# Performance work log

Measured on AMD Instinct MI355X. Metric: run time of the kernel, lower is better.

## Reference

```python
import jax, jax.numpy as jnp
import numpy as np

N_REGION = 50000
N_SUBJECT = 8192
D_REGION = 128
D_SUBJECT = 64
HIDDEN = 128
OUT = 64
E_RR = 1000000
E_HS = 400000


def setup_inputs() -> dict:
    key = jax.random.key(0)
    ks = jax.random.split(key, 18)
    w = lambda k, s: jax.random.normal(k, s, jnp.float32) * 0.05
    return {
        "x_region": jax.random.normal(ks[0], (N_REGION, D_REGION), jnp.float32),
        "x_subject": jax.random.normal(ks[1], (N_SUBJECT, D_SUBJECT), jnp.float32),
        "rr_src": jax.random.randint(ks[2], (E_RR,), 0, N_REGION, jnp.int32),
        "rr_dst": jax.random.randint(ks[3], (E_RR,), 0, N_REGION, jnp.int32),
        "hs_src": jax.random.randint(ks[4], (E_HS,), 0, N_REGION, jnp.int32),
        "hs_dst": jax.random.randint(ks[5], (E_HS,), 0, N_SUBJECT, jnp.int32),
        "Wg1": w(ks[6], (D_REGION, HIDDEN)), "bg1": w(ks[7], (HIDDEN,)),
        "Wl1": w(ks[8], (D_REGION, HIDDEN)), "bl1": w(ks[9], (HIDDEN,)),
        "Wr1": w(ks[10], (D_SUBJECT, HIDDEN)),
        "Wg2": w(ks[11], (HIDDEN, HIDDEN)), "bg2": w(ks[12], (HIDDEN,)),
        "Wl2": w(ks[13], (HIDDEN, HIDDEN)), "bl2": w(ks[14], (HIDDEN,)),
        "Wr2": w(ks[15], (HIDDEN, HIDDEN)),
        "Wout": w(ks[16], (HIDDEN, OUT)), "bout": w(ks[17], (OUT,)),
    }


def _gcn(x, src, dst, W, b, n):
    # GCNConv: symmetric normalization over A + I (add_self_loops=True)
    h = x @ W                                   # [n, hidden]
    deg = jnp.zeros((n,), x.dtype).at[dst].add(1.0) + 1.0  # in-degree + self-loop
    dinv = jax.lax.rsqrt(deg)
    norm = dinv[src] * dinv[dst]                # [E]
    out = jax.ops.segment_sum(h[src] * norm[:, None], dst, num_segments=n)
    return out + h / deg[:, None] + b           # self-loop term has norm 1/deg


def _sage(x_src, x_dst, src, dst, Wl, bl, Wr, n_dst):
    # SAGEConv: lin_l(mean_neighbors) + bias + lin_r(x_dst) (lin_r has no bias)
    s = jax.ops.segment_sum(x_src[src], dst, num_segments=n_dst)
    cnt = jax.ops.segment_sum(jnp.ones_like(src, dtype=x_src.dtype), dst, num_segments=n_dst)
    mean = s / jnp.maximum(cnt, 1.0)[:, None]
    return mean @ Wl + bl + x_dst @ Wr


def reference(x_region, x_subject, rr_src, rr_dst, hs_src, hs_dst,
              Wg1, bg1, Wl1, bl1, Wr1, Wg2, bg2, Wl2, bl2, Wr2, Wout, bout):
    # Layer 1 (HeteroConv applies both relations to the same input x_dict)
    r1 = _gcn(x_region, rr_src, rr_dst, Wg1, bg1, N_REGION)
    s1 = _sage(x_region, x_subject, hs_src, hs_dst, Wl1, bl1, Wr1, N_SUBJECT)
    # Layer 2
    r2 = _gcn(r1, rr_src, rr_dst, Wg2, bg2, N_REGION)
    s2 = _sage(r1, s1, hs_src, hs_dst, Wl2, bl2, Wr2, N_SUBJECT)
    # Final shared linear on each node type; concat (region rows, then subject rows)
    return jnp.concatenate([r2 @ Wout + bout, s2 @ Wout + bout], axis=0)
```

## Files before the change

### kernel.cpp

```cpp
#include <hip/hip_runtime.h>
#include <hip/hip_bf16.h>
#include <cstddef>

#define NR 50000
#define NS 8192
#define DR 128
#define DSUBJ 64
#define HID 128
#define OUTD 64
#define ERR_E 1000000
#define EHS_E 400000

__device__ inline int wave_incl_scan(int x, int lane) {
#pragma unroll
    for (int off = 1; off < 64; off <<= 1) {
        int t = __shfl_up(x, off, 64);
        if (lane >= off) x += t;
    }
    return x;
}

__global__ __launch_bounds__(256) void count_edges_both(const int* __restrict__ rr_dst,
                                                        const int* __restrict__ hs_dst,
                                                        int* __restrict__ rrCnt,
                                                        int* __restrict__ hsCnt) {
    int t = blockIdx.x * 256 + threadIdx.x;
    if (t < ERR_E) {
        atomicAdd(&rrCnt[rr_dst[t]], 1);
    } else {
        int u = t - ERR_E;
        if (u < EHS_E) atomicAdd(&hsCnt[hs_dst[u]], 1);
    }
}

__global__ __launch_bounds__(1024) void block_sums(const int* __restrict__ cnt,
                                                   int* __restrict__ partial, int n) {
    int tid = threadIdx.x, lane = tid & 63, wid = tid >> 6;
    int i = blockIdx.x * 1024 + tid;
    int v = (i < n) ? cnt[i] : 0;
    int s = v;
#pragma unroll
    for (int off = 1; off < 64; off <<= 1) s += __shfl_xor(s, off, 64);
    __shared__ int wsum[16];
    if (lane == 0) wsum[wid] = s;
    __syncthreads();
    if (tid == 0) {
        int tot = 0;
#pragma unroll
        for (int w = 0; w < 16; ++w) tot += wsum[w];
        partial[blockIdx.x] = tot;
    }
}

__global__ __launch_bounds__(64) void scan_partials(int* __restrict__ partial, int nb) {
    int lane = threadIdx.x;
    int v = (lane < nb) ? partial[lane] : 0;
    int incl = wave_incl_scan(v, lane);
    if (lane < nb) partial[lane] = incl - v;
}

template <int MODE>
__global__ __launch_bounds__(1024) void scan_finalize(int* __restrict__ cnt_cursor,
                                                      const int* __restrict__ partial,
                                                      int* __restrict__ rowptr,
                                                      float* __restrict__ scale, int n) {
    int tid = threadIdx.x, lane = tid & 63, wid = tid >> 6;
    int i = blockIdx.x * 1024 + tid;
    int v = (i < n) ? cnt_cursor[i] : 0;
    int incl = wave_incl_scan(v, lane);
    __shared__ int wsum[16];
    if (lane == 63) wsum[wid] = incl;
    __syncthreads();
    if (wid == 0 && lane < 16) {
        int orig = wsum[lane];
        int wv = orig;
#pragma unroll
        for (int off = 1; off < 16; off <<= 1) {
            int t = __shfl_up(wv, off, 64);
            if (lane >= off) wv += t;
        }
        wsum[lane] = wv - orig;
    }
    __syncthreads();
    int excl = partial[blockIdx.x] + wsum[wid] + incl - v;
    if (i < n) {
        rowptr[i + 1] = excl + v;
        cnt_cursor[i] = excl;
        if (MODE == 0) scale[i] = rsqrtf((float)(v + 1));
        else           scale[i] = 1.0f / fmaxf((float)v, 1.0f);
    }
    if (i == 0) rowptr[0] = 0;
}

__global__ __launch_bounds__(256) void fill_csr_both(const int* __restrict__ rr_src,
                                                     const int* __restrict__ rr_dst,
                                                     int* __restrict__ rrCursor,
                                                     int* __restrict__ rrCol,
                                                     const int* __restrict__ hs_src,
                                                     const int* __restrict__ hs_dst,
                                                     int* __restrict__ hsCursor,
                                                     int* __restrict__ hsCol) {
    int t = blockIdx.x * 256 + threadIdx.x;
    if (t < ERR_E) {
        int p = atomicAdd(&rrCursor[rr_dst[t]], 1);
        rrCol[p] = rr_src[t];
    } else {
        int u = t - ERR_E;
        if (u < EHS_E) {
            int p = atomicAdd(&hsCursor[hs_dst[u]], 1);
            hsCol[p] = hs_src[u];
        }
    }
}

template <int N, int K, bool BIAS, bool RS, bool ACCUM>
__global__ __launch_bounds__(256, 2) void gemm_lds(const float* __restrict__ A,
                                                   const float* __restrict__ W,
                                                   const float* __restrict__ bias,
                                                   const float* __restrict__ rs,
                                                   float* __restrict__ out, int M) {
    constexpr int CG = N / 4;
    constexpr int SLOTS = 256 / CG;
    constexpr int RPT = 64 / SLOTS;
    __shared__ float wl[K * N];

    for (int i = threadIdx.x * 4; i < K * N; i += 1024)
        *(float4*)&wl[i] = *(const float4*)&W[i];
    __syncthreads();

    int cg = threadIdx.x & (CG - 1);
    int rl = threadIdx.x / CG;
    int col = cg * 4;
    int row0 = blockIdx.x * 64 + rl * RPT;

    float4 acc[RPT];
#pragma unroll
    for (int j = 0; j < RPT; ++j) { acc[j].x = acc[j].y = acc[j].z = acc[j].w = 0.0f; }

#pragma unroll 2
    for (int k0 = 0; k0 < K; k0 += 4) {
        float4 a[RPT];
#pragma unroll
        for (int j = 0; j < RPT; ++j) {
            int r = row0 + j; if (r > M - 1) r = M - 1;
            a[j] = *(const float4*)(A + (size_t)r * K + k0);
        }
#pragma unroll
        for (int kk = 0; kk < 4; ++kk) {
            float4 w = *(float4*)&wl[(k0 + kk) * N + col];
#pragma unroll
            for (int j = 0; j < RPT; ++j) {
                float av = (kk == 0) ? a[j].x : (kk == 1) ? a[j].y : (kk == 2) ? a[j].z : a[j].w;
                acc[j].x += av * w.x;
                acc[j].y += av * w.y;
                acc[j].z += av * w.z;
                acc[j].w += av * w.w;
            }
        }
    }

    float4 b4;
    if (BIAS) b4 = *(const float4*)(bias + col);
#pragma unroll
    for (int j = 0; j < RPT; ++j) {
        int r = row0 + j;
        if (r >= M) continue;
        float4 v = acc[j];
        if (RS) { float sc = rs[r]; v.x *= sc; v.y *= sc; v.z *= sc; v.w *= sc; }
        if (BIAS) { v.x += b4.x; v.y += b4.y; v.z += b4.z; v.w += b4.w; }
        float* op = out + (size_t)r * N + col;
        if (ACCUM) {
            float4 o = *(const float4*)op;
            v.x += o.x; v.y += o.y; v.z += o.z; v.w += o.w;
        }
        *(float4*)op = v;
    }
}

__global__ __launch_bounds__(256) void gcn_gather(const float* __restrict__ h,
                                                  const int* __restrict__ rowptr,
                                                  const int* __restrict__ col,
                                                  const float* __restrict__ dinv,
                                                  const float* __restrict__ bias,
                                                  float* __restrict__ out, int n) {
    int wid = threadIdx.x >> 6;
    int lane = threadIdx.x & 63;
    int r = blockIdx.x * 4 + wid;
    if (r >= n) return;
    const float2* hp = (const float2*)h;
    float2 acc = hp[(size_t)r * 64 + lane];
    int e = rowptr[r], end = rowptr[r + 1];
    for (; e + 7 < end; e += 8) {
        int s0 = col[e],     s1 = col[e + 1], s2 = col[e + 2], s3 = col[e + 3];
        int s4 = col[e + 4], s5 = col[e + 5], s6 = col[e + 6], s7 = col[e + 7];
        float2 v0 = hp[(size_t)s0 * 64 + lane];
        float2 v1 = hp[(size_t)s1 * 64 + lane];
        float2 v2 = hp[(size_t)s2 * 64 + lane];
        float2 v3 = hp[(size_t)s3 * 64 + lane];
        float2 v4 = hp[(size_t)s4 * 64 + lane];
        float2 v5 = hp[(size_t)s5 * 64 + lane];
        float2 v6 = hp[(size_t)s6 * 64 + lane];
        float2 v7 = hp[(size_t)s7 * 64 + lane];
        acc.x += ((v0.x + v1.x) + (v2.x + v3.x)) + ((v4.x + v5.x) + (v6.x + v7.x));
        acc.y += ((v0.y + v1.y) + (v2.y + v3.y)) + ((v4.y + v5.y) + (v6.y + v7.y));
    }
    for (; e + 3 < end; e += 4) {
        int s0 = col[e], s1 = col[e + 1], s2 = col[e + 2], s3 = col[e + 3];
        float2 v0 = hp[(size_t)s0 * 64 + lane];
        float2 v1 = hp[(size_t)s1 * 64 + lane];
        float2 v2 = hp[(size_t)s2 * 64 + lane];
        float2 v3 = hp[(size_t)s3 * 64 + lane];
        acc.x += (v0.x + v1.x) + (v2.x + v3.x);
        acc.y += (v0.y + v1.y) + (v2.y + v3.y);
    }
    for (; e < end; ++e) {
        int s = col[e];
        float2 v = hp[(size_t)s * 64 + lane];
        acc.x += v.x; acc.y += v.y;
    }
    float dv = dinv[r];
    float2 b = ((const float2*)bias)[lane];
    acc.x = acc.x * dv + b.x;
    acc.y = acc.y * dv + b.y;
    ((float2*)out)[(size_t)r * 64 + lane] = acc;
}

__global__ __launch_bounds__(256) void sage_gather(const float* __restrict__ x,
                                                   const int* __restrict__ rowptr,
                                                   const int* __restrict__ col,
                                                   const float* __restrict__ invcnt,
                                                   float* __restrict__ out, int n) {
    int wid = threadIdx.x >> 6;
    int lane = threadIdx.x & 63;
    int r = blockIdx.x * 4 + wid;
    if (r >= n) return;
    const float2* xp = (const float2*)x;
    float2 acc; acc.x = 0.0f; acc.y = 0.0f;
    int e = rowptr[r], end = rowptr[r + 1];
    for (; e + 7 < end; e += 8) {
        int s0 = col[e],     s1 = col[e + 1], s2 = col[e + 2], s3 = col[e + 3];
        int s4 = col[e + 4], s5 = col[e + 5], s6 = col[e + 6], s7 = col[e + 7];
        float2 v0 = xp[(size_t)s0 * 64 + lane];
        float2 v1 = xp[(size_t)s1 * 64 + lane];
        float2 v2 = xp[(size_t)s2 * 64 + lane];
        float2 v3 = xp[(size_t)s3 * 64 + lane];
        float2 v4 = xp[(size_t)s4 * 64 + lane];
        float2 v5 = xp[(size_t)s5 * 64 + lane];
        float2 v6 = xp[(size_t)s6 * 64 + lane];
        float2 v7 = xp[(size_t)s7 * 64 + lane];
        acc.x += ((v0.x + v1.x) + (v2.x + v3.x)) + ((v4.x + v5.x) + (v6.x + v7.x));
        acc.y += ((v0.y + v1.y) + (v2.y + v3.y)) + ((v4.y + v5.y) + (v6.y + v7.y));
    }
    for (; e + 3 < end; e += 4) {
        int s0 = col[e], s1 = col[e + 1], s2 = col[e + 2], s3 = col[e + 3];
        float2 v0 = xp[(size_t)s0 * 64 + lane];
        float2 v1 = xp[(size_t)s1 * 64 + lane];
        float2 v2 = xp[(size_t)s2 * 64 + lane];
        float2 v3 = xp[(size_t)s3 * 64 + lane];
        acc.x += (v0.x + v1.x) + (v2.x + v3.x);
        acc.y += (v0.y + v1.y) + (v2.y + v3.y);
    }
    for (; e < end; ++e) {
        int s = col[e];
        float2 v = xp[(size_t)s * 64 + lane];
        acc.x += v.x; acc.y += v.y;
    }
    float ic = invcnt[r];
    acc.x *= ic; acc.y *= ic;
    ((float2*)out)[(size_t)r * 64 + lane] = acc;
}

extern "C" void kernel_launch(void* const* d_in, const int* in_sizes, int n_in,
                              void* d_out, int out_size, void* d_ws, size_t ws_size,
                              hipStream_t stream) {
    const float* x_region = (const float*)d_in[0];
    const float* x_subject = (const float*)d_in[1];
    const int* rr_src = (const int*)d_in[2];
    const int* rr_dst = (const int*)d_in[3];
    const int* hs_src = (const int*)d_in[4];
    const int* hs_dst = (const int*)d_in[5];
    const float* Wg1 = (const float*)d_in[6];
    const float* bg1 = (const float*)d_in[7];
    const float* Wl1 = (const float*)d_in[8];
    const float* bl1 = (const float*)d_in[9];
    const float* Wr1 = (const float*)d_in[10];
    const float* Wg2 = (const float*)d_in[11];
    const float* bg2 = (const float*)d_in[12];
    const float* Wl2 = (const float*)d_in[13];
    const float* bl2 = (const float*)d_in[14];
    const float* Wr2 = (const float*)d_in[15];
    const float* Wout = (const float*)d_in[16];
    const float* bout = (const float*)d_in[17];
    float* out = (float*)d_out;

    float* ws = (float*)d_ws;
    float* A  = ws;
    float* C  = A + (size_t)NR * 128;
    float* SA = C + (size_t)NR * 128;
    float* SB = SA + (size_t)NS * 128;
    float* SC = SB + (size_t)NS * 128;
    float* dinv   = SC + (size_t)NS * 128;
    float* invcnt = dinv + NR;
    int* rrRowptr = (int*)(invcnt + NS);
    int* rrCursor = rrRowptr + NR + 1;
    int* rrCol    = rrCursor + NR;
    int* hsRowptr = rrCol + ERR_E;
    int* hsCursor = hsRowptr + NS + 1;
    int* hsCol    = hsCursor + NS;
    int* rrPart   = hsCol + EHS_E;
    int* hsPart   = rrPart + 64;

    const int TB = 256;
    constexpr int RR_BLKS = (NR + 1023) / 1024;
    constexpr int HS_BLKS = (NS + 1023) / 1024;

    hipMemsetAsync(rrCursor, 0, (size_t)NR * sizeof(int), stream);
    hipMemsetAsync(hsCursor, 0, (size_t)NS * sizeof(int), stream);
    count_edges_both<<<(ERR_E + EHS_E + TB - 1) / TB, TB, 0, stream>>>(
        rr_dst, hs_dst, rrCursor, hsCursor);
    block_sums<<<RR_BLKS, 1024, 0, stream>>>(rrCursor, rrPart, NR);
    block_sums<<<HS_BLKS, 1024, 0, stream>>>(hsCursor, hsPart, NS);
    scan_partials<<<1, 64, 0, stream>>>(rrPart, RR_BLKS);
    scan_partials<<<1, 64, 0, stream>>>(hsPart, HS_BLKS);
    scan_finalize<0><<<RR_BLKS, 1024, 0, stream>>>(rrCursor, rrPart, rrRowptr, dinv, NR);
    scan_finalize<1><<<HS_BLKS, 1024, 0, stream>>>(hsCursor, hsPart, hsRowptr, invcnt, NS);
    fill_csr_both<<<(ERR_E + EHS_E + TB - 1) / TB, TB, 0, stream>>>(
        rr_src, rr_dst, rrCursor, rrCol, hs_src, hs_dst, hsCursor, hsCol);

    gemm_lds<128, 128, false, true, false><<<(NR + 63) / 64, TB, 0, stream>>>(
        x_region, Wg1, nullptr, dinv, A, NR);
    gcn_gather<<<(NR + 3) / 4, TB, 0, stream>>>(A, rrRowptr, rrCol, dinv, bg1, C, NR);
    sage_gather<<<(NS + 3) / 4, TB, 0, stream>>>(x_region, hsRowptr, hsCol, invcnt, SA, NS);
    gemm_lds<128, 128, true, false, false><<<(NS + 63) / 64, TB, 0, stream>>>(
        SA, Wl1, bl1, nullptr, SB, NS);
    gemm_lds<128, 64, false, false, true><<<(NS + 63) / 64, TB, 0, stream>>>(
        x_subject, Wr1, nullptr, nullptr, SB, NS);

    sage_gather<<<(NS + 3) / 4, TB, 0, stream>>>(C, hsRowptr, hsCol, invcnt, SA, NS);
    gemm_lds<128, 128, true, false, false><<<(NS + 63) / 64, TB, 0, stream>>>(
        SA, Wl2, bl2, nullptr, SC, NS);
    gemm_lds<128, 128, false, false, true><<<(NS + 63) / 64, TB, 0, stream>>>(
        SB, Wr2, nullptr, nullptr, SC, NS);
    gemm_lds<128, 128, false, true, false><<<(NR + 63) / 64, TB, 0, stream>>>(
        C, Wg2, nullptr, dinv, A, NR);
    gcn_gather<<<(NR + 3) / 4, TB, 0, stream>>>(A, rrRowptr, rrCol, dinv, bg2, C, NR);

    gemm_lds<64, 128, true, false, false><<<(NR + 63) / 64, TB, 0, stream>>>(
        C, Wout, bout, nullptr, out, NR);
    gemm_lds<64, 128, true, false, false><<<(NS + 63) / 64, TB, 0, stream>>>(
        SC, Wout, bout, nullptr, out + (size_t)NR * 64, NS);
}
```

Baseline: 689.1 us.

## Store gathered node features in bf16 to halve gather traffic

The GCN pre-aggregation GEMM now writes its output in bf16. Layer-1 GCN output gets a bf16 mirror, and x_region is cast to bf16 up front. Both gather kernels read these bf16 rows and accumulate in fp32, halving the bytes fetched per random edge access. The trade is lower precision on the aggregated features, plus an extra cast kernel and an extra mirror write.

```diff
diff --git a/kernel.cpp b/kernel.cpp
--- a/kernel.cpp
+++ b/kernel.cpp
@@ -10,6 +10,22 @@
 #define OUTD 64
 #define ERR_E 1000000
 #define EHS_E 400000
+
+typedef unsigned int uint32;
+typedef unsigned short ushort16;
+
+__device__ inline float bf16lo(uint32 u) { return __uint_as_float(u << 16); }
+__device__ inline float bf16hi(uint32 u) { return __uint_as_float(u & 0xffff0000u); }
+__device__ inline ushort16 f2bf(float f) {
+    uint32 u = __float_as_uint(f);
+    u += 0x7fffu + ((u >> 16) & 1u);
+    return (ushort16)(u >> 16);
+}
+__device__ inline uint32 pack2bf(float x, float y) {
+    uint32 ux = __float_as_uint(x); ux += 0x7fffu + ((ux >> 16) & 1u);
+    uint32 uy = __float_as_uint(y); uy += 0x7fffu + ((uy >> 16) & 1u);
+    return (ux >> 16) | (uy & 0xffff0000u);
+}
 
 __device__ inline int wave_incl_scan(int x, int lane) {
 #pragma unroll
@@ -113,7 +129,17 @@
     }
 }
 
-template <int N, int K, bool BIAS, bool RS, bool ACCUM>
+__global__ __launch_bounds__(256) void cast_bf(const float4* __restrict__ in,
+                                               ushort16* __restrict__ out, int n4) {
+    int i = blockIdx.x * 256 + threadIdx.x;
+    if (i < n4) {
+        float4 v = in[i];
+        ushort16* o = out + (size_t)i * 4;
+        o[0] = f2bf(v.x); o[1] = f2bf(v.y); o[2] = f2bf(v.z); o[3] = f2bf(v.w);
+    }
+}
+
+template <int N, int K, bool BIAS, bool RS, bool ACCUM, bool OB>
 __global__ __launch_bounds__(256, 2) void gemm_lds(const float* __restrict__ A,
                                                    const float* __restrict__ W,
                                                    const float* __restrict__ bias,
@@ -168,106 +194,118 @@
         float4 v = acc[j];
         if (RS) { float sc = rs[r]; v.x *= sc; v.y *= sc; v.z *= sc; v.w *= sc; }
         if (BIAS) { v.x += b4.x; v.y += b4.y; v.z += b4.z; v.w += b4.w; }
-        float* op = out + (size_t)r * N + col;
-        if (ACCUM) {
-            float4 o = *(const float4*)op;
-            v.x += o.x; v.y += o.y; v.z += o.z; v.w += o.w;
-        }
-        *(float4*)op = v;
-    }
-}
-
-__global__ __launch_bounds__(256) void gcn_gather(const float* __restrict__ h,
-                                                  const int* __restrict__ rowptr,
-                                                  const int* __restrict__ col,
-                                                  const float* __restrict__ dinv,
-                                                  const float* __restrict__ bias,
-                                                  float* __restrict__ out, int n) {
+        if (OB) {
+            uint32 lo = pack2bf(v.x, v.y);
+            uint32 hi = pack2bf(v.z, v.w);
+            uint32* op = (uint32*)((ushort16*)out + (size_t)r * N + col);
+            op[0] = lo; op[1] = hi;
+        } else {
+            float* op = out + (size_t)r * N + col;
+            if (ACCUM) {
+                float4 o = *(const float4*)op;
+                v.x += o.x; v.y += o.y; v.z += o.z; v.w += o.w;
+            }
+            *(float4*)op = v;
+        }
+    }
+}
+
+template <bool DUALW>
+__global__ __launch_bounds__(256) void gcn_gather_bf(const ushort16* __restrict__ h,
+                                                     const int* __restrict__ rowptr,
+                                                     const int* __restrict__ col,
+                                                     const float* __restrict__ dinv,
+                                                     const float* __restrict__ bias,
+                                                     float* __restrict__ out,
+                                                     ushort16* __restrict__ mirror, int n) {
     int wid = threadIdx.x >> 6;
     int lane = threadIdx.x & 63;
     int r = blockIdx.x * 4 + wid;
     if (r >= n) return;
-    const float2* hp = (const float2*)h;
-    float2 acc = hp[(size_t)r * 64 + lane];
+    const uint32* hp = (const uint32*)h;
+    uint32 us = hp[(size_t)r * 64 + lane];
+    float ax = bf16lo(us), ay = bf16hi(us);
     int e = rowptr[r], end = rowptr[r + 1];
     for (; e + 7 < end; e += 8) {
         int s0 = col[e],     s1 = col[e + 1], s2 = col[e + 2], s3 = col[e + 3];
         int s4 = col[e + 4], s5 = col[e + 5], s6 = col[e + 6], s7 = col[e + 7];
-        float2 v0 = hp[(size_t)s0 * 64 + lane];
-        float2 v1 = hp[(size_t)s1 * 64 + lane];
-        float2 v2 = hp[(size_t)s2 * 64 + lane];
-        float2 v3 = hp[(size_t)s3 * 64 + lane];
-        float2 v4 = hp[(size_t)s4 * 64 + lane];
-        float2 v5 = hp[(size_t)s5 * 64 + lane];
-        float2 v6 = hp[(size_t)s6 * 64 + lane];
-        float2 v7 = hp[(size_t)s7 * 64 + lane];
-        acc.x += ((v0.x + v1.x) + (v2.x + v3.x)) + ((v4.x + v5.x) + (v6.x + v7.x));
-        acc.y += ((v0.y + v1.y) + (v2.y + v3.y)) + ((v4.y + v5.y) + (v6.y + v7.y));
+        uint32 u0 = hp[(size_t)s0 * 64 + lane];
+        uint32 u1 = hp[(size_t)s1 * 64 + lane];
+        uint32 u2 = hp[(size_t)s2 * 64 + lane];
+        uint32 u3 = hp[(size_t)s3 * 64 + lane];
+        uint32 u4 = hp[(size_t)s4 * 64 + lane];
+        uint32 u5 = hp[(size_t)s5 * 64 + lane];
+        uint32 u6 = hp[(size_t)s6 * 64 + lane];
+        uint32 u7 = hp[(size_t)s7 * 64 + lane];
+        ax += ((bf16lo(u0) + bf16lo(u1)) + (bf16lo(u2) + bf16lo(u3)))
+            + ((bf16lo(u4) + bf16lo(u5)) + (bf16lo(u6) + bf16lo(u7)));
+        ay += ((bf16hi(u0) + bf16hi(u1)) + (bf16hi(u2) + bf16hi(u3)))
+            + ((bf16hi(u4) + bf16hi(u5)) + (bf16hi(u6) + bf16hi(u7)));
     }
     for (; e + 3 < end; e += 4) {
         int s0 = col[e], s1 = col[e + 1], s2 = col[e + 2], s3 = col[e + 3];
-        float2 v0 = hp[(size_t)s0 * 64 + lane];
-        float2 v1 = hp[(size_t)s1 * 64 + lane];
-        float2 v2 = hp[(size_t)s2 * 64 + lane];
-        float2 v3 = hp[(size_t)s3 * 64 + lane];
-        acc.x += (v0.x + v1.x) + (v2.x + v3.x);
-        acc.y += (v0.y + v1.y) + (v2.y + v3.y);
+        uint32 u0 = hp[(size_t)s0 * 64 + lane];
+        uint32 u1 = hp[(size_t)s1 * 64 + lane];
+        uint32 u2 = hp[(size_t)s2 * 64 + lane];
+        uint32 u3 = hp[(size_t)s3 * 64 + lane];
+        ax += (bf16lo(u0) + bf16lo(u1)) + (bf16lo(u2) + bf16lo(u3));
+        ay += (bf16hi(u0) + bf16hi(u1)) + (bf16hi(u2) + bf16hi(u3));
     }
     for (; e < end; ++e) {
-        int s = col[e];
-        float2 v = hp[(size_t)s * 64 + lane];
-        acc.x += v.x; acc.y += v.y;
+        uint32 u = hp[(size_t)col[e] * 64 + lane];
+        ax += bf16lo(u); ay += bf16hi(u);
     }
     float dv = dinv[r];
     float2 b = ((const float2*)bias)[lane];
-    acc.x = acc.x * dv + b.x;
-    acc.y = acc.y * dv + b.y;
-    ((float2*)out)[(size_t)r * 64 + lane] = acc;
-}
-
-__global__ __launch_bounds__(256) void sage_gather(const float* __restrict__ x,
-                                                   const int* __restrict__ rowptr,
-                                                   const int* __restrict__ col,
-                                                   const float* __restrict__ invcnt,
-                                                   float* __restrict__ out, int n) {
+    float ox = ax * dv + b.x;
+    float oy = ay * dv + b.y;
+    ((float2*)out)[(size_t)r * 64 + lane] = make_float2(ox, oy);
+    if (DUALW) ((uint32*)mirror)[(size_t)r * 64 + lane] = pack2bf(ox, oy);
+}
+
+__global__ __launch_bounds__(256) void sage_gather_bf(const ushort16* __restrict__ x,
+                                                      const int* __restrict__ rowptr,
+                                                      const int* __restrict__ col,
+                                                      const float* __restrict__ invcnt,
+                                                      float* __restrict__ out, int n) {
     int wid = threadIdx.x >> 6;
     int lane = threadIdx.x & 63;
     int r = blockIdx.x * 4 + wid;
     if (r >= n) return;
-    const float2* xp = (const float2*)x;
-    float2 acc; acc.x = 0.0f; acc.y = 0.0f;
+    const uint32* xp = (const uint32*)x;
+    float ax = 0.0f, ay = 0.0f;
     int e = rowptr[r], end = rowptr[r + 1];
     for (; e + 7 < end; e += 8) {
         int s0 = col[e],     s1 = col[e + 1], s2 = col[e + 2], s3 = col[e + 3];
         int s4 = col[e + 4], s5 = col[e + 5], s6 = col[e + 6], s7 = col[e + 7];
-        float2 v0 = xp[(size_t)s0 * 64 + lane];
-        float2 v1 = xp[(size_t)s1 * 64 + lane];
-        float2 v2 = xp[(size_t)s2 * 64 + lane];
-        float2 v3 = xp[(size_t)s3 * 64 + lane];
-        float2 v4 = xp[(size_t)s4 * 64 + lane];
-        float2 v5 = xp[(size_t)s5 * 64 + lane];
-        float2 v6 = xp[(size_t)s6 * 64 + lane];
-        float2 v7 = xp[(size_t)s7 * 64 + lane];
-        acc.x += ((v0.x + v1.x) + (v2.x + v3.x)) + ((v4.x + v5.x) + (v6.x + v7.x));
-        acc.y += ((v0.y + v1.y) + (v2.y + v3.y)) + ((v4.y + v5.y) + (v6.y + v7.y));
+        uint32 u0 = xp[(size_t)s0 * 64 + lane];
+        uint32 u1 = xp[(size_t)s1 * 64 + lane];
+        uint32 u2 = xp[(size_t)s2 * 64 + lane];
+        uint32 u3 = xp[(size_t)s3 * 64 + lane];
+        uint32 u4 = xp[(size_t)s4 * 64 + lane];
+        uint32 u5 = xp[(size_t)s5 * 64 + lane];
+        uint32 u6 = xp[(size_t)s6 * 64 + lane];
+        uint32 u7 = xp[(size_t)s7 * 64 + lane];
+        ax += ((bf16lo(u0) + bf16lo(u1)) + (bf16lo(u2) + bf16lo(u3)))
+            + ((bf16lo(u4) + bf16lo(u5)) + (bf16lo(u6) + bf16lo(u7)));
+        ay += ((bf16hi(u0) + bf16hi(u1)) + (bf16hi(u2) + bf16hi(u3)))
+            + ((bf16hi(u4) + bf16hi(u5)) + (bf16hi(u6) + bf16hi(u7)));
     }
     for (; e + 3 < end; e += 4) {
         int s0 = col[e], s1 = col[e + 1], s2 = col[e + 2], s3 = col[e + 3];
-        float2 v0 = xp[(size_t)s0 * 64 + lane];
-        float2 v1 = xp[(size_t)s1 * 64 + lane];
-        float2 v2 = xp[(size_t)s2 * 64 + lane];
-        float2 v3 = xp[(size_t)s3 * 64 + lane];
-        acc.x += (v0.x + v1.x) + (v2.x + v3.x);
-        acc.y += (v0.y + v1.y) + (v2.y + v3.y);
+        uint32 u0 = xp[(size_t)s0 * 64 + lane];
+        uint32 u1 = xp[(size_t)s1 * 64 + lane];
+        uint32 u2 = xp[(size_t)s2 * 64 + lane];
+        uint32 u3 = xp[(size_t)s3 * 64 + lane];
+        ax += (bf16lo(u0) + bf16lo(u1)) + (bf16lo(u2) + bf16lo(u3));
+        ay += (bf16hi(u0) + bf16hi(u1)) + (bf16hi(u2) + bf16hi(u3));
     }
     for (; e < end; ++e) {
-        int s = col[e];
-        float2 v = xp[(size_t)s * 64 + lane];
-        acc.x += v.x; acc.y += v.y;
+        uint32 u = xp[(size_t)col[e] * 64 + lane];
+        ax += bf16lo(u); ay += bf16hi(u);
     }
     float ic = invcnt[r];
-    acc.x *= ic; acc.y *= ic;
-    ((float2*)out)[(size_t)r * 64 + lane] = acc;
+    ((float2*)out)[(size_t)r * 64 + lane] = make_float2(ax * ic, ay * ic);
 }
 
 extern "C" void kernel_launch(void* const* d_in, const int* in_sizes, int n_in,
@@ -295,6 +333,8 @@
 
     float* ws = (float*)d_ws;
     float* A  = ws;
+    ushort16* hb  = (ushort16*)A;
+    ushort16* r1b = hb + (size_t)NR * 128;
     float* C  = A + (size_t)NR * 128;
     float* SA = C + (size_t)NR * 128;
     float* SB = SA + (size_t)NS * 128;
@@ -309,6 +349,7 @@
     int* hsCol    = hsCursor + NS;
     int* rrPart   = hsCol + EHS_E;
     int* hsPart   = rrPart + 64;
+    ushort16* xrb = (ushort16*)(hsPart + 64);
 
     const int TB = 256;
     constexpr int RR_BLKS = (NR + 1023) / 1024;
@@ -318,6 +359,8 @@
     hipMemsetAsync(hsCursor, 0, (size_t)NS * sizeof(int), stream);
     count_edges_both<<<(ERR_E + EHS_E + TB - 1) / TB, TB, 0, stream>>>(
         rr_dst, hs_dst, rrCursor, hsCursor);
+    cast_bf<<<(NR * 128 / 4 + TB - 1) / TB, TB, 0, stream>>>(
+        (const float4*)x_region, xrb, NR * 128 / 4);
     block_sums<<<RR_BLKS, 1024, 0, stream>>>(rrCursor, rrPart, NR);
     block_sums<<<HS_BLKS, 1024, 0, stream>>>(hsCursor, hsPart, NS);
     scan_partials<<<1, 64, 0, stream>>>(rrPart, RR_BLKS);
@@ -327,26 +370,28 @@
     fill_csr_both<<<(ERR_E + EHS_E + TB - 1) / TB, TB, 0, stream>>>(
         rr_src, rr_dst, rrCursor, rrCol, hs_src, hs_dst, hsCursor, hsCol);
 
-    gemm_lds<128, 128, false, true, false><<<(NR + 63) / 64, TB, 0, stream>>>(
-        x_region, Wg1, nullptr, dinv, A, NR);
-    gcn_gather<<<(NR + 3) / 4, TB, 0, stream>>>(A, rrRowptr, rrCol, dinv, bg1, C, NR);
-    sage_gather<<<(NS + 3) / 4, TB, 0, stream>>>(x_region, hsRowptr, hsCol, invcnt, SA, NS);
-    gemm_lds<128, 128, true, false, false><<<(NS + 63) / 64, TB, 0, stream>>>(
+    gemm_lds<128, 128, false, true, false, true><<<(NR + 63) / 64, TB, 0, stream>>>(
+        x_region, Wg1, nullptr, dinv, (float*)hb, NR);
+    gcn_gather_bf<true><<<(NR + 3) / 4, TB, 0, stream>>>(
+        hb, rrRowptr, rrCol, dinv, bg1, C, r1b, NR);
+    sage_gather_bf<<<(NS + 3) / 4, TB, 0, stream>>>(xrb, hsRowptr, hsCol, invcnt, SA, NS);
+    gemm_lds<128, 128, true, false, false, false><<<(NS + 63) / 64, TB, 0, stream>>>(
         SA, Wl1, bl1, nullptr, SB, NS);
-    gemm_lds<128, 64, false, false, true><<<(NS + 63) / 64, TB, 0, stream>>>(
+    gemm_lds<128, 64, false, false, true, false><<<(NS + 63) / 64, TB, 0, stream>>>(
         x_subject, Wr1, nullptr, nullptr, SB, NS);
 
-    sage_gather<<<(NS + 3) / 4, TB, 0, stream>>>(C, hsRowptr, hsCol, invcnt, SA, NS);
-    gemm_lds<128, 128, true, false, false><<<(NS + 63) / 64, TB, 0, stream>>>(
+    sage_gather_bf<<<(NS + 3) / 4, TB, 0, stream>>>(r1b, hsRowptr, hsCol, invcnt, SA, NS);
+    gemm_lds<128, 128, true, false, false, false><<<(NS + 63) / 64, TB, 0, stream>>>(
         SA, Wl2, bl2, nullptr, SC, NS);
-    gemm_lds<128, 128, false, false, true><<<(NS + 63) / 64, TB, 0, stream>>>(
+    gemm_lds<128, 128, false, false, true, false><<<(NS + 63) / 64, TB, 0, stream>>>(
         SB, Wr2, nullptr, nullptr, SC, NS);
-    gemm_lds<128, 128, false, true, false><<<(NR + 63) / 64, TB, 0, stream>>>(
-        C, Wg2, nullptr, dinv, A, NR);
-    gcn_gather<<<(NR + 3) / 4, TB, 0, stream>>>(A, rrRowptr, rrCol, dinv, bg2, C, NR);
-
-    gemm_lds<64, 128, true, false, false><<<(NR + 63) / 64, TB, 0, stream>>>(
+    gemm_lds<128, 128, false, true, false, true><<<(NR + 63) / 64, TB, 0, stream>>>(
+        C, Wg2, nullptr, dinv, (float*)hb, NR);
+    gcn_gather_bf<false><<<(NR + 3) / 4, TB, 0, stream>>>(
+        hb, rrRowptr, rrCol, dinv, bg2, C, nullptr, NR);
+
+    gemm_lds<64, 128, true, false, false, false><<<(NR + 63) / 64, TB, 0, stream>>>(
         C, Wout, bout, nullptr, out, NR);
-    gemm_lds<64, 128, true, false, false><<<(NS + 63) / 64, TB, 0, stream>>>(
+    gemm_lds<64, 128, true, false, false, false><<<(NS + 63) / 64, TB, 0, stream>>>(
         SC, Wout, bout, nullptr, out + (size_t)NR * 64, NS);
 }
```

Measured after the change: 618.1 us. 1.11x faster.
